# Kernel tuning notes

Measured on AMD Instinct MI355X. Metric: run time of the kernel, lower is better.

The kernel has to match this reference:

```python
import jax, jax.numpy as jnp
import numpy as np

N = 8          # num_tasks (PHQ-8)
D_EMB = 64     # task_embed_dim
HID = 128      # hidden_dim
L = 2          # num_gat_layers
H = 4          # num_heads
B = 16384      # batch size

CLUSTERS = {'core_depression': [0, 1, 5], 'cognitive': [6, 7], 'somatic': [2, 3, 4]}
CROSS = [(0, 6), (0, 7), (1, 6), (1, 7), (5, 6), (5, 7), (0, 2), (0, 3), (1, 2), (1, 3), (1, 4), (6, 2), (7, 3)]


def build_graph():
    adj = np.eye(N, dtype=np.int32)
    et = np.zeros((N, N), dtype=np.int32)
    for idxs in CLUSTERS.values():
        for i in idxs:
            for j in idxs:
                adj[i, j] = 1
                if i != j:
                    et[i, j] = 1
    for i, j in CROSS:
        adj[i, j] = 1
        adj[j, i] = 1
        et[i, j] = 2
        et[j, i] = 2
    return adj, et


def setup_inputs() -> dict:
    key = jax.random.key(0)
    ks = jax.random.split(key, 10)
    adj, et = build_graph()
    s = 0.05
    return {
        'shared_embedding': jax.random.normal(ks[0], (B, HID), dtype=jnp.float32),
        'task_embeddings': jax.random.normal(ks[1], (N, D_EMB), dtype=jnp.float32) * s,
        'W_in': jax.random.normal(ks[2], (HID, D_EMB), dtype=jnp.float32) * s,
        'b_in': jnp.zeros((HID,), dtype=jnp.float32),
        'W_heads': jax.random.normal(ks[3], (L, H, HID, HID), dtype=jnp.float32) * s,
        'a_heads': jax.random.normal(ks[4], (L, H, 2 * HID), dtype=jnp.float32) * s,
        'out_W': jax.random.normal(ks[5], (L, HID, H * HID), dtype=jnp.float32) * s,
        'out_b': jnp.zeros((L, HID), dtype=jnp.float32),
        'ln_scale': jnp.ones((L, HID), dtype=jnp.float32),
        'ln_bias': jnp.zeros((L, HID), dtype=jnp.float32),
        'omega_intra': jnp.asarray(1.0, dtype=jnp.float32),
        'omega_cross': jnp.asarray(0.6, dtype=jnp.float32),
        'adj': jnp.asarray(adj),
        'edge_types': jnp.asarray(et),
    }


def reference(shared_embedding, task_embeddings, W_in, b_in, W_heads, a_heads,
              out_W, out_b, ln_scale, ln_bias, omega_intra, omega_cross, adj, edge_types):
    adjf = adj.astype(jnp.float32)
    # learnable edge weights: intra-cluster omega_intra, cross-cluster omega_cross, zero off-edge
    ew = jnp.ones_like(adjf)
    ew = jnp.where(edge_types == 1, omega_intra, ew)
    ew = jnp.where(edge_types == 2, omega_cross, ew)
    ew = ew * adjf  # [N, N]

    b = shared_embedding.shape[0]
    h_task = task_embeddings @ W_in.T + b_in          # [N, HID]
    h = h_task[None, :, :] + shared_embedding[:, None, :]  # [B, N, HID]

    n_layers = W_heads.shape[0]
    for l in range(n_layers):
        # per-head projection: Linear(y = x W^T), W_heads[l]: [H, out, in]
        Wh = jnp.einsum('bnf,hgf->bhng', h, W_heads[l])  # [B, H, N, F]
        f = Wh.shape[-1]
        a_src = a_heads[l][:, :f]   # [H, F]
        a_dst = a_heads[l][:, f:]   # [H, F]
        # concat-based additive score decomposed into two dot products
        ei = jnp.einsum('bhnf,hf->bhn', Wh, a_src)
        ej = jnp.einsum('bhnf,hf->bhn', Wh, a_dst)
        e = jax.nn.leaky_relu(ei[:, :, :, None] + ej[:, :, None, :], 0.2)  # [B,H,N,N]
        att = jnp.where(adjf[None, None] > 0, e, jnp.float32(-9e15))
        # faithful to original: masked entries multiplied by (zero) edge weights -> 0 logits
        att = att * ew[None, None]
        att = jax.nn.softmax(att, axis=-1)
        hp = jax.nn.elu(jnp.einsum('bhnm,bhmf->bhnf', att, Wh))  # [B,H,N,F]
        hcat = jnp.moveaxis(hp, 1, 2).reshape(b, hp.shape[2], -1)  # [B,N,H*F]
        gout = hcat @ out_W[l].T + out_b[l]  # [B,N,HID]
        # residual + layernorm
        x = h + gout
        mu = x.mean(-1, keepdims=True)
        var = x.var(-1, keepdims=True)
        h = (x - mu) / jnp.sqrt(var + 1e-5) * ln_scale[l] + ln_bias[l]
    return h, ew
```

## Files before the change

kernel.cpp:

```cpp
#include <hip/hip_runtime.h>
#include <stdint.h>

typedef __attribute__((ext_vector_type(8))) short bf16x8;
typedef __attribute__((ext_vector_type(4))) float f32x4;
typedef unsigned long long ull;

typedef uint4 uint4_a __attribute__((may_alias));
typedef ull ull_a __attribute__((may_alias));
typedef bf16x8 bf16x8_a __attribute__((may_alias));
typedef f32x4 f32x4_a __attribute__((may_alias));

#define LGKM0() __builtin_amdgcn_s_waitcnt(0xc07f)
#define MFMA16(a, b, c) __builtin_amdgcn_mfma_f32_16x16x32_bf16((a), (b), (c), 0, 0, 0)

__device__ __forceinline__ unsigned f2bf(float x) {
    unsigned u = __float_as_uint(x);
    return (u + 0x7fffu + ((u >> 16) & 1u)) >> 16;
}
__device__ __forceinline__ float bf2f(short s) {
    return __uint_as_float(((unsigned)(unsigned short)s) << 16);
}
__device__ __forceinline__ ull pack4(f32x4 v) {
    return (ull)f2bf(v.x) | ((ull)f2bf(v.y) << 16) | ((ull)f2bf(v.z) << 32) | ((ull)f2bf(v.w) << 48);
}

__global__ void gat_prep(const float* __restrict__ te, const float* __restrict__ W_in,
                         const float* __restrict__ b_in, const float* __restrict__ W_heads,
                         const float* __restrict__ a_heads, const float* __restrict__ om_i,
                         const float* __restrict__ om_c, const int* __restrict__ adj,
                         const int* __restrict__ et, const float* __restrict__ out_W,
                         unsigned short* __restrict__ wsWf, unsigned short* __restrict__ wsWsd,
                         float* __restrict__ wsHt, float* __restrict__ wsEw,
                         float* __restrict__ eout) {
    const int gid = blockIdx.x, tid = threadIdx.x;
    if (gid < 1024) {
        int idx = gid * 256 + tid;
        int j = idx & 7, lane = (idx >> 3) & 63, frag = (idx >> 9) & 31, chunk = idx >> 14;
        int cc = lane & 15, qq = lane >> 4, kk = frag >> 3, t = frag & 7;
        int l = chunk >> 3, h = (chunk >> 1) & 3;
        float v;
        if (chunk & 1)
            v = out_W[(l * 128 + 16 * t + cc) * 512 + 128 * h + 32 * kk + 8 * qq + j];
        else
            v = W_heads[((l * 4 + h) * 128 + 16 * t + cc) * 128 + 32 * kk + 8 * qq + j];
        wsWf[idx] = (unsigned short)f2bf(v);
    } else if (gid < 1056) {
        const int grp = tid >> 3, sg = tid & 7;
        const int idx = (gid - 1024) * 32 + grp;
        const int n = idx >> 7, o = idx & 127;
        const float4 t0 = *(const float4*)(te + n * 64 + 8 * sg);
        const float4 t1 = *(const float4*)(te + n * 64 + 8 * sg + 4);
        const float4 w0 = *(const float4*)(W_in + o * 64 + 8 * sg);
        const float4 w1 = *(const float4*)(W_in + o * 64 + 8 * sg + 4);
        float s = t0.x * w0.x + t0.y * w0.y + t0.z * w0.z + t0.w * w0.w +
                  t1.x * w1.x + t1.y * w1.y + t1.z * w1.z + t1.w * w1.w;
        s += __shfl_xor(s, 1);
        s += __shfl_xor(s, 2);
        s += __shfl_xor(s, 4);
        if (sg == 0) wsHt[idx] = s + b_in[o];
    } else if (gid < 1184) {
        const int grp = tid >> 3, sg = tid & 7;
        const int idx = (gid - 1056) * 32 + grp;
        const int l = idx >> 11, p = (idx >> 7) & 15, f = idx & 127;
        float s = 0.f;
        if (p < 8) {
            const int hh = p >> 1, ss = p & 1;
            const float* a = a_heads + (l * 4 + hh) * 256 + ss * 128;
            const float* Wb = W_heads + (l * 4 + hh) * 16384;
#pragma unroll
            for (int gg = 0; gg < 16; ++gg) {
                const int g = 16 * sg + gg;
                s += a[g] * Wb[g * 128 + f];
            }
        }
        s += __shfl_xor(s, 1);
        s += __shfl_xor(s, 2);
        s += __shfl_xor(s, 4);
        if (sg == 0) wsWsd[idx] = (unsigned short)f2bf(s);
    } else {
        if (tid < 64) {
            float v = 0.f;
            if (adj[tid]) {
                int t = et[tid];
                v = (t == 1) ? om_i[0] : ((t == 2) ? om_c[0] : 1.0f);
            }
            wsEw[tid] = v;
            eout[tid] = v;
        }
    }
}

__global__ __launch_bounds__(256, 2) void gat_main(
    const float* __restrict__ shared_emb, const float* __restrict__ out_b,
    const float* __restrict__ ln_s, const float* __restrict__ ln_b,
    const unsigned short* __restrict__ wsWf, const unsigned short* __restrict__ wsWsd,
    const float* __restrict__ wsHt, const float* __restrict__ wsEw, float* __restrict__ out) {
    __shared__ __align__(16) unsigned short sScr[4][5120];
    __shared__ __align__(16) float sE[4][32][8];
    __shared__ __align__(16) unsigned short sAtt[4][32][8];

    const int tid = threadIdx.x;
    const int w = tid >> 6, lane = tid & 63, q = lane >> 4, c = lane & 15;
    const long wrow0 = (long)blockIdx.x * 128 + (long)w * 32;

    bf16x8 xf[2][4];
#pragma unroll
    for (int mt = 0; mt < 2; ++mt) {
        const long row = wrow0 + 16 * mt + c;
        const size_t b = (size_t)(row >> 3);
        const int t = (int)(row & 7);
#pragma unroll
        for (int kk = 0; kk < 4; ++kk) {
            const int f0 = 32 * kk + 8 * q;
            const float4 s0 = *(const float4*)(shared_emb + b * 128 + f0);
            const float4 s1 = *(const float4*)(shared_emb + b * 128 + f0 + 4);
            const float4 h0 = *(const float4*)(wsHt + t * 128 + f0);
            const float4 h1 = *(const float4*)(wsHt + t * 128 + f0 + 4);
            float v[8] = {s0.x + h0.x, s0.y + h0.y, s0.z + h0.z, s0.w + h0.w,
                          s1.x + h1.x, s1.y + h1.y, s1.z + h1.z, s1.w + h1.w};
            bf16x8 r;
#pragma unroll
            for (int j = 0; j < 8; ++j) r[j] = (short)f2bf(v[j]);
            xf[mt][kk] = r;
        }
    }

    f32x4 gacc[8][2];

    for (int chunk = 0; chunk < 16; ++chunk) {
        const int l = chunk >> 3, h = (chunk >> 1) & 3, isW2 = chunk & 1;
        const unsigned short* __restrict__ wf = wsWf + (size_t)chunk * 16384 + (size_t)lane * 8;
        if (!isW2) {
            if (h == 0) {
                const f32x4 z4 = {0.f, 0.f, 0.f, 0.f};
#pragma unroll
                for (int ot = 0; ot < 8; ++ot)
#pragma unroll
                    for (int nt = 0; nt < 2; ++nt) gacc[ot][nt] = z4;
                f32x4 e[2] = {z4, z4};
#pragma unroll
                for (int kk = 0; kk < 4; ++kk) {
                    bf16x8 bw = *(const bf16x8_a*)(wsWsd + ((l << 4) + c) * 128 + 32 * kk + 8 * q);
#pragma unroll
                    for (int mt = 0; mt < 2; ++mt) e[mt] = MFMA16(xf[mt][kk], bw, e[mt]);
                }
                if (c < 8) {
#pragma unroll
                    for (int mt = 0; mt < 2; ++mt)
#pragma unroll
                        for (int r = 0; r < 4; ++r) sE[w][16 * mt + 4 * q + r][c] = e[mt][r];
                }
                LGKM0();
            }
            if (lane < 32) {
                const int r = lane, eb = r & 24;
                const float ei = sE[w][r][2 * h];
                float lgt[8];
#pragma unroll
                for (int m = 0; m < 8; ++m) {
                    float s = ei + sE[w][eb + m][2 * h + 1];
                    s = s > 0.f ? s : 0.2f * s;
                    lgt[m] = s * wsEw[(r & 7) * 8 + m];
                }
                float mx = lgt[0];
#pragma unroll
                for (int m = 1; m < 8; ++m) mx = fmaxf(mx, lgt[m]);
                float p[8], sum = 0.f;
#pragma unroll
                for (int m = 0; m < 8; ++m) {
                    p[m] = __expf(lgt[m] - mx);
                    sum += p[m];
                }
                const float inv = 1.0f / sum;
                uint4 av;
                av.x = f2bf(p[0] * inv) | (f2bf(p[1] * inv) << 16);
                av.y = f2bf(p[2] * inv) | (f2bf(p[3] * inv) << 16);
                av.z = f2bf(p[4] * inv) | (f2bf(p[5] * inv) << 16);
                av.w = f2bf(p[6] * inv) | (f2bf(p[7] * inv) << 16);
                *(uint4_a*)&sAtt[w][r][0] = av;
            }
            LGKM0();

            f32x4 acc[16];
            {
                const f32x4 z4 = {0.f, 0.f, 0.f, 0.f};
#pragma unroll
                for (int i = 0; i < 16; ++i) acc[i] = z4;
            }
#pragma unroll
            for (int kk = 0; kk < 4; ++kk)
#pragma unroll
                for (int gt = 0; gt < 8; ++gt) {
                    bf16x8 bw = *(const bf16x8_a*)(wf + (size_t)(kk * 8 + gt) * 512);
#pragma unroll
                    for (int mt = 0; mt < 2; ++mt)
                        acc[mt * 8 + gt] = MFMA16(xf[mt][kk], bw, acc[mt * 8 + gt]);
                }
#pragma unroll
            for (int gt = 0; gt < 8; ++gt)
#pragma unroll
                for (int mt = 0; mt < 2; ++mt)
                    *(ull_a*)&sScr[w][(16 * gt + c) * 40 + 16 * mt + 4 * q] =
                        pack4(acc[mt * 8 + gt]);
            LGKM0();
            bf16x8 bat[2];
#pragma unroll
            for (int nt = 0; nt < 2; ++nt) {
                const int n = 16 * nt + c;
                bf16x8 zb;
#pragma unroll
                for (int j = 0; j < 8; ++j) zb[j] = 0;
                bat[nt] = (q == 2 * nt + (c >> 3)) ? *(const bf16x8_a*)&sAtt[w][n][0] : zb;
            }
            {
                const f32x4 z4 = {0.f, 0.f, 0.f, 0.f};
#pragma unroll
                for (int i = 0; i < 16; ++i) acc[i] = z4;
            }
#pragma unroll
            for (int ct = 0; ct < 8; ++ct) {
                bf16x8 a0 = *(const bf16x8_a*)&sScr[w][(16 * ct + c) * 40 + 8 * q];
#pragma unroll
                for (int nt = 0; nt < 2; ++nt)
                    acc[ct * 2 + nt] = MFMA16(a0, bat[nt], acc[ct * 2 + nt]);
            }
            LGKM0();
#pragma unroll
            for (int ct = 0; ct < 8; ++ct)
#pragma unroll
                for (int nt = 0; nt < 2; ++nt) {
                    f32x4 v = acc[ct * 2 + nt];
#pragma unroll
                    for (int j = 0; j < 4; ++j) {
                        float x = v[j];
                        v[j] = x > 0.f ? x : (__expf(x) - 1.f);
                    }
                    *(ull_a*)&sScr[w][(16 * nt + c) * 136 + 16 * ct + 4 * q] = pack4(v);
                }
            LGKM0();
        } else {
#pragma unroll
            for (int kk = 0; kk < 4; ++kk) {
                bf16x8 bh[2];
#pragma unroll
                for (int nt = 0; nt < 2; ++nt)
                    bh[nt] = *(const bf16x8_a*)&sScr[w][(16 * nt + c) * 136 + 32 * kk + 8 * q];
#pragma unroll
                for (int ot = 0; ot < 8; ++ot) {
                    bf16x8 aw = *(const bf16x8_a*)(wf + (size_t)(kk * 8 + ot) * 512);
#pragma unroll
                    for (int nt = 0; nt < 2; ++nt) gacc[ot][nt] = MFMA16(aw, bh[nt], gacc[ot][nt]);
                }
            }
            if (h == 3) {
                LGKM0();
                float* sF = (float*)&sScr[w][0];
                const float* ob = out_b + l * 128;
                const float* lsc = ln_s + l * 128;
                const float* lbi = ln_b + l * 128;
#pragma unroll
                for (int nt = 0; nt < 2; ++nt) {
#pragma unroll
                    for (int ot = 0; ot < 8; ++ot)
                        *(f32x4_a*)&sF[c * 132 + 16 * ot + 4 * q] = gacc[ot][nt];
                    LGKM0();
                    float sum = 0.f, ssq = 0.f;
#pragma unroll
                    for (int kk = 0; kk < 4; ++kk) {
                        const int f0 = 32 * kk + 8 * q;
                        f32x4 g0 = *(const f32x4_a*)&sF[c * 132 + f0];
                        f32x4 g1 = *(const f32x4_a*)&sF[c * 132 + f0 + 4];
                        bf16x8 x8 = xf[nt][kk];
#pragma unroll
                        for (int j = 0; j < 4; ++j) {
                            float x = g0[j] + bf2f(x8[j]) + ob[f0 + j];
                            sum += x;
                            ssq += x * x;
                            float x2 = g1[j] + bf2f(x8[4 + j]) + ob[f0 + 4 + j];
                            sum += x2;
                            ssq += x2 * x2;
                        }
                    }
                    sum += __shfl_xor(sum, 16);
                    sum += __shfl_xor(sum, 32);
                    ssq += __shfl_xor(ssq, 16);
                    ssq += __shfl_xor(ssq, 32);
                    const float mu = sum * (1.0f / 128.0f);
                    const float var = ssq * (1.0f / 128.0f) - mu * mu;
                    const float rs = rsqrtf(var + 1e-5f);
#pragma unroll
                    for (int kk = 0; kk < 4; ++kk) {
                        const int f0 = 32 * kk + 8 * q;
                        f32x4 g0 = *(const f32x4_a*)&sF[c * 132 + f0];
                        f32x4 g1 = *(const f32x4_a*)&sF[c * 132 + f0 + 4];
                        bf16x8 x8 = xf[nt][kk];
                        float y[8];
#pragma unroll
                        for (int j = 0; j < 4; ++j) {
                            float x = g0[j] + bf2f(x8[j]) + ob[f0 + j];
                            y[j] = (x - mu) * rs * lsc[f0 + j] + lbi[f0 + j];
                            float x2 = g1[j] + bf2f(x8[4 + j]) + ob[f0 + 4 + j];
                            y[4 + j] = (x2 - mu) * rs * lsc[f0 + 4 + j] + lbi[f0 + 4 + j];
                        }
                        if (l == 0) {
                            bf16x8 r;
#pragma unroll
                            for (int j = 0; j < 8; ++j) r[j] = (short)f2bf(y[j]);
                            xf[nt][kk] = r;
                        } else {
                            f32x4 o0 = {y[0], y[1], y[2], y[3]};
                            f32x4 o1 = {y[4], y[5], y[6], y[7]};
                            *(f32x4_a*)&sF[c * 132 + f0] = o0;
                            *(f32x4_a*)&sF[c * 132 + f0 + 4] = o1;
                        }
                    }
                    if (l == 1) {
                        LGKM0();
#pragma unroll
                        for (int i = 0; i < 8; ++i) {
                            const int flat = i * 256 + lane * 4;
                            const int rr = flat >> 7, c0 = flat & 127;
                            f32x4 v = *(const f32x4_a*)&sF[rr * 132 + c0];
                            *(f32x4_a*)(out + (size_t)(wrow0 + 16 * nt + rr) * 128 + c0) = v;
                        }
                    }
                    LGKM0();
                }
            }
        }
    }
}

extern "C" void kernel_launch(void* const* d_in, const int* in_sizes, int n_in, void* d_out,
                              int out_size, void* d_ws, size_t ws_size, hipStream_t stream) {
    const float* shared_emb = (const float*)d_in[0];
    const float* te = (const float*)d_in[1];
    const float* W_in = (const float*)d_in[2];
    const float* b_in = (const float*)d_in[3];
    const float* W_heads = (const float*)d_in[4];
    const float* a_heads = (const float*)d_in[5];
    const float* out_W = (const float*)d_in[6];
    const float* out_b = (const float*)d_in[7];
    const float* ln_s = (const float*)d_in[8];
    const float* ln_b = (const float*)d_in[9];
    const float* om_i = (const float*)d_in[10];
    const float* om_c = (const float*)d_in[11];
    const int* adj = (const int*)d_in[12];
    const int* et = (const int*)d_in[13];
    float* out = (float*)d_out;

    unsigned short* wsWf = (unsigned short*)d_ws;
    unsigned short* wsWsd = wsWf + 262144;
    float* wsHt = (float*)((char*)d_ws + 532480);
    float* wsEw = wsHt + 1024;

    float* eout = out + (out_size - 64);

    gat_prep<<<1185, 256, 0, stream>>>(te, W_in, b_in, W_heads, a_heads, om_i, om_c, adj, et,
                                       out_W, wsWf, wsWsd, wsHt, wsEw, eout);

    const int B = in_sizes[0] / 128;
    const int grid = (B * 8) / 128;
    gat_main<<<grid, 256, 0, stream>>>(shared_emb, out_b, ln_s, ln_b, wsWf, wsWsd, wsHt, wsEw,
                                       out);
}
```

Baseline: 371.6 us.

## Feed projection accumulators directly into attention MFMA, skipping LDS round-trip

The per-head projection accumulators are packed to bf16 in registers and used straight as the A operand of a 16x16x16 MFMA against the attention matrix. This removes the LDS write, wait and re-read of the projected features, and it processes the heads in two halves to lower register pressure. Scheduling barriers are placed after each LDS wait so the compiler cannot hoist work across them, which may also limit instruction overlap. The scratch LDS buffer shrinks accordingly.

```diff
diff --git a/kernel.cpp b/kernel.cpp
--- a/kernel.cpp
+++ b/kernel.cpp
@@ -2,15 +2,18 @@
 #include <stdint.h>
 
 typedef __attribute__((ext_vector_type(8))) short bf16x8;
+typedef __attribute__((ext_vector_type(4))) short bf16x4;
 typedef __attribute__((ext_vector_type(4))) float f32x4;
 typedef unsigned long long ull;
 
 typedef uint4 uint4_a __attribute__((may_alias));
 typedef ull ull_a __attribute__((may_alias));
 typedef bf16x8 bf16x8_a __attribute__((may_alias));
+typedef bf16x4 bf16x4_a __attribute__((may_alias));
 typedef f32x4 f32x4_a __attribute__((may_alias));
 
 #define LGKM0() __builtin_amdgcn_s_waitcnt(0xc07f)
+#define SBAR0() __builtin_amdgcn_sched_barrier(0)
 #define MFMA16(a, b, c) __builtin_amdgcn_mfma_f32_16x16x32_bf16((a), (b), (c), 0, 0, 0)
 
 __device__ __forceinline__ unsigned f2bf(float x) {
@@ -22,6 +25,25 @@
 }
 __device__ __forceinline__ ull pack4(f32x4 v) {
     return (ull)f2bf(v.x) | ((ull)f2bf(v.y) << 16) | ((ull)f2bf(v.z) << 32) | ((ull)f2bf(v.w) << 48);
+}
+__device__ __forceinline__ bf16x4 pkA(f32x4 v) {
+    bf16x4 r;
+    r[0] = (short)f2bf(v.x);
+    r[1] = (short)f2bf(v.y);
+    r[2] = (short)f2bf(v.z);
+    r[3] = (short)f2bf(v.w);
+    return r;
+}
+__device__ __forceinline__ f32x4 MFMA16K16(bf16x4 a, bf16x4 b, f32x4 c) {
+#if defined(__HIP_DEVICE_COMPILE__)
+#if __has_builtin(__builtin_amdgcn_mfma_f32_16x16x16bf16_1k)
+    return __builtin_amdgcn_mfma_f32_16x16x16bf16_1k(a, b, c, 0, 0, 0);
+#else
+    return __builtin_amdgcn_mfma_f32_16x16x16_bf16(a, b, c, 0, 0, 0);
+#endif
+#else
+    return c;
+#endif
 }
 
 __global__ void gat_prep(const float* __restrict__ te, const float* __restrict__ W_in,
@@ -95,7 +117,7 @@
     const float* __restrict__ ln_s, const float* __restrict__ ln_b,
     const unsigned short* __restrict__ wsWf, const unsigned short* __restrict__ wsWsd,
     const float* __restrict__ wsHt, const float* __restrict__ wsEw, float* __restrict__ out) {
-    __shared__ __align__(16) unsigned short sScr[4][5120];
+    __shared__ __align__(16) unsigned short sScr[4][4352];
     __shared__ __align__(16) float sE[4][32][8];
     __shared__ __align__(16) unsigned short sAtt[4][32][8];
 
@@ -151,6 +173,7 @@
                         for (int r = 0; r < 4; ++r) sE[w][16 * mt + 4 * q + r][c] = e[mt][r];
                 }
                 LGKM0();
+                SBAR0();
             }
             if (lane < 32) {
                 const int r = lane, eb = r & 24;
@@ -180,64 +203,53 @@
                 *(uint4_a*)&sAtt[w][r][0] = av;
             }
             LGKM0();
-
-            f32x4 acc[16];
-            {
-                const f32x4 z4 = {0.f, 0.f, 0.f, 0.f};
-#pragma unroll
-                for (int i = 0; i < 16; ++i) acc[i] = z4;
-            }
-#pragma unroll
-            for (int kk = 0; kk < 4; ++kk)
-#pragma unroll
-                for (int gt = 0; gt < 8; ++gt) {
-                    bf16x8 bw = *(const bf16x8_a*)(wf + (size_t)(kk * 8 + gt) * 512);
-#pragma unroll
-                    for (int mt = 0; mt < 2; ++mt)
-                        acc[mt * 8 + gt] = MFMA16(xf[mt][kk], bw, acc[mt * 8 + gt]);
-                }
-#pragma unroll
-            for (int gt = 0; gt < 8; ++gt)
-#pragma unroll
-                for (int mt = 0; mt < 2; ++mt)
-                    *(ull_a*)&sScr[w][(16 * gt + c) * 40 + 16 * mt + 4 * q] =
-                        pack4(acc[mt * 8 + gt]);
+            SBAR0();
+
+            const f32x4 z4 = {0.f, 0.f, 0.f, 0.f};
+#pragma unroll
+            for (int half = 0; half < 2; ++half) {
+                f32x4 acc[8];
+#pragma unroll
+                for (int i = 0; i < 8; ++i) acc[i] = z4;
+#pragma unroll
+                for (int kk = 0; kk < 4; ++kk)
+#pragma unroll
+                    for (int g2 = 0; g2 < 4; ++g2) {
+                        const int gt = 4 * half + g2;
+                        bf16x8 bw = *(const bf16x8_a*)(wf + (size_t)(kk * 8 + gt) * 512);
+#pragma unroll
+                        for (int mt = 0; mt < 2; ++mt)
+                            acc[mt * 4 + g2] = MFMA16(xf[mt][kk], bw, acc[mt * 4 + g2]);
+                    }
+                bf16x4 pa[8];
+#pragma unroll
+                for (int i = 0; i < 8; ++i) pa[i] = pkA(acc[i]);
+                f32x4 hpt[8];
+#pragma unroll
+                for (int nt = 0; nt < 2; ++nt) {
+                    bf16x4 bat = {0, 0, 0, 0};
+                    if ((q >> 1) == (c >> 3))
+                        bat = *(const bf16x4_a*)&sAtt[w][16 * nt + c][4 * (q & 1)];
+#pragma unroll
+                    for (int g2 = 0; g2 < 4; ++g2)
+                        hpt[g2 * 2 + nt] = MFMA16K16(pa[nt * 4 + g2], bat, z4);
+                }
+#pragma unroll
+                for (int g2 = 0; g2 < 4; ++g2)
+#pragma unroll
+                    for (int nt = 0; nt < 2; ++nt) {
+                        const int gt = 4 * half + g2;
+                        f32x4 v = hpt[g2 * 2 + nt];
+#pragma unroll
+                        for (int j = 0; j < 4; ++j) {
+                            float x = v[j];
+                            v[j] = x > 0.f ? x : (__expf(x) - 1.f);
+                        }
+                        *(ull_a*)&sScr[w][(16 * nt + c) * 136 + 16 * gt + 4 * q] = pack4(v);
+                    }
+            }
             LGKM0();
-            bf16x8 bat[2];
-#pragma unroll
-            for (int nt = 0; nt < 2; ++nt) {
-                const int n = 16 * nt + c;
-                bf16x8 zb;
-#pragma unroll
-                for (int j = 0; j < 8; ++j) zb[j] = 0;
-                bat[nt] = (q == 2 * nt + (c >> 3)) ? *(const bf16x8_a*)&sAtt[w][n][0] : zb;
-            }
-            {
-                const f32x4 z4 = {0.f, 0.f, 0.f, 0.f};
-#pragma unroll
-                for (int i = 0; i < 16; ++i) acc[i] = z4;
-            }
-#pragma unroll
-            for (int ct = 0; ct < 8; ++ct) {
-                bf16x8 a0 = *(const bf16x8_a*)&sScr[w][(16 * ct + c) * 40 + 8 * q];
-#pragma unroll
-                for (int nt = 0; nt < 2; ++nt)
-                    acc[ct * 2 + nt] = MFMA16(a0, bat[nt], acc[ct * 2 + nt]);
-            }
-            LGKM0();
-#pragma unroll
-            for (int ct = 0; ct < 8; ++ct)
-#pragma unroll
-                for (int nt = 0; nt < 2; ++nt) {
-                    f32x4 v = acc[ct * 2 + nt];
-#pragma unroll
-                    for (int j = 0; j < 4; ++j) {
-                        float x = v[j];
-                        v[j] = x > 0.f ? x : (__expf(x) - 1.f);
-                    }
-                    *(ull_a*)&sScr[w][(16 * nt + c) * 136 + 16 * ct + 4 * q] = pack4(v);
-                }
-            LGKM0();
+            SBAR0();
         } else {
 #pragma unroll
             for (int kk = 0; kk < 4; ++kk) {
@@ -254,6 +266,7 @@
             }
             if (h == 3) {
                 LGKM0();
+                SBAR0();
                 float* sF = (float*)&sScr[w][0];
                 const float* ob = out_b + l * 128;
                 const float* lsc = ln_s + l * 128;
@@ -264,6 +277,7 @@
                     for (int ot = 0; ot < 8; ++ot)
                         *(f32x4_a*)&sF[c * 132 + 16 * ot + 4 * q] = gacc[ot][nt];
                     LGKM0();
+                    SBAR0();
                     float sum = 0.f, ssq = 0.f;
 #pragma unroll
                     for (int kk = 0; kk < 4; ++kk) {
@@ -316,6 +330,7 @@
                     }
                     if (l == 1) {
                         LGKM0();
+                        SBAR0();
 #pragma unroll
                         for (int i = 0; i < 8; ++i) {
                             const int flat = i * 256 + lane * 4;
@@ -325,6 +340,7 @@
                         }
                     }
                     LGKM0();
+                    SBAR0();
                 }
             }
         }
```

Result: faster. 309.9 us (-16.6%).
